# Optimization experiments

Hardware: AMD Instinct MI355X
Metric: run time of the kernel (lower is better)

Reference implementation:

```python
import jax, jax.numpy as jnp
import numpy as np

B, NF, NT = 8, 4096, 4096
D_IN, D_HID, D_OUT, D_V = 3, 128, 32, 16


def mlp(x, W1, b1, W2, b2):
    # x: [B, N, D_IN] -> [B, N, D_OUT]
    h = jax.nn.relu(jnp.einsum('bni,ih->bnh', x, W1) + b1)
    return jnp.einsum('bnh,ho->bno', h, W2) + b2


def l1_cdist(a, b):
    # a: [B, N, d], b: [B, M, d] -> [B, N, M], sum_d |a-b|
    # scan over the small feature dim d to avoid a [B,N,M,d] intermediate
    aT = jnp.moveaxis(a, -1, 0)  # [d, B, N]
    bT = jnp.moveaxis(b, -1, 0)  # [d, B, M]

    def step(acc, ab):
        ai, bi = ab
        return acc + jnp.abs(ai[:, :, None] - bi[:, None, :]), None

    init = jnp.zeros((a.shape[0], a.shape[1], b.shape[1]), dtype=a.dtype)
    acc, _ = jax.lax.scan(step, init, (aT, bT))
    return acc


def setup_inputs() -> dict:
    key = jax.random.key(0)
    ks = jax.random.split(key, 11)
    s1 = 1.0 / np.sqrt(D_IN)
    s2 = 1.0 / np.sqrt(D_HID)
    return {
        'coords_f': jax.random.normal(ks[0], (B, NF, D_IN), jnp.float32),
        'values_f': jax.random.normal(ks[1], (B, NF, D_V), jnp.float32),
        'coords_t': jax.random.normal(ks[2], (B, NT, D_IN), jnp.float32),
        'Wk1': jax.random.uniform(ks[3], (D_IN, D_HID), jnp.float32, -s1, s1),
        'bk1': jax.random.uniform(ks[4], (D_HID,), jnp.float32, -s1, s1),
        'Wk2': jax.random.uniform(ks[5], (D_HID, D_OUT), jnp.float32, -s2, s2),
        'bk2': jax.random.uniform(ks[6], (D_OUT,), jnp.float32, -s2, s2),
        'Wq1': jax.random.uniform(ks[7], (D_IN, D_HID), jnp.float32, -s1, s1),
        'bq1': jax.random.uniform(ks[8], (D_HID,), jnp.float32, -s1, s1),
        'Wq2': jax.random.uniform(ks[9], (D_HID, D_OUT), jnp.float32, -s2, s2),
        'bq2': jax.random.uniform(ks[10], (D_OUT,), jnp.float32, -s2, s2),
    }


def reference(coords_f, values_f, coords_t, Wk1, bk1, Wk2, bk2, Wq1, bq1, Wq2, bq2):
    Wk = mlp(coords_f, Wk1, bk1, Wk2, bk2)  # [B, NF, D_OUT]
    Wq = mlp(coords_t, Wq1, bq1, Wq2, bq2)  # [B, NT, D_OUT]
    score = l1_cdist(Wk, Wq)                # [B, NF, NT]
    attn = jax.nn.softmax(-(score ** 2) / 2.0, axis=1)  # softmax over NF
    # 'bij,bik->bjk': [B,NF,NT] x [B,NF,V] -> [B,NT,V]
    return jnp.einsum('bij,bik->bjk', attn, values_f)
```

## Files before the change

kernel.cpp:

```cpp
#include <hip/hip_runtime.h>

#define B 8
#define NF 4096
#define NT 4096
#define D_HID 128
#define D_OUT 32
#define D_V 16
#define TILE_I 64

__device__ inline float fast_exp2(float x) {
#if __has_builtin(__builtin_amdgcn_exp2f)
  return __builtin_amdgcn_exp2f(x);
#else
  return exp2f(x);
#endif
}

__global__ __launch_bounds__(256) void mlp_kernel(
    const float* __restrict__ x, const float* __restrict__ W1,
    const float* __restrict__ b1, const float* __restrict__ W2,
    const float* __restrict__ b2, float* __restrict__ out) {
  __shared__ float sW1[3 * D_HID];
  __shared__ float sb1[D_HID];
  __shared__ float sW2[D_HID * D_OUT];
  __shared__ float sb2[D_OUT];
  const int tid = threadIdx.x;
  for (int idx = tid; idx < D_HID * D_OUT; idx += 256) sW2[idx] = W2[idx];
  for (int idx = tid; idx < 3 * D_HID; idx += 256) sW1[idx] = W1[idx];
  if (tid < D_HID) sb1[tid] = b1[tid];
  if (tid < D_OUT) sb2[tid] = b2[tid];
  __syncthreads();

  const int t = blockIdx.x * 256 + tid;
  const float x0 = x[t * 3 + 0];
  const float x1 = x[t * 3 + 1];
  const float x2 = x[t * 3 + 2];
  float acc[D_OUT];
#pragma unroll
  for (int o = 0; o < D_OUT; ++o) acc[o] = sb2[o];
#pragma unroll 4
  for (int h = 0; h < D_HID; ++h) {
    float hv = fmaf(x2, sW1[2 * D_HID + h],
               fmaf(x1, sW1[1 * D_HID + h],
               fmaf(x0, sW1[0 * D_HID + h], sb1[h])));
    hv = fmaxf(hv, 0.0f);
    const float4* w2r = reinterpret_cast<const float4*>(&sW2[h * D_OUT]);
#pragma unroll
    for (int o4 = 0; o4 < D_OUT / 4; ++o4) {
      const float4 w = w2r[o4];
      acc[o4 * 4 + 0] = fmaf(hv, w.x, acc[o4 * 4 + 0]);
      acc[o4 * 4 + 1] = fmaf(hv, w.y, acc[o4 * 4 + 1]);
      acc[o4 * 4 + 2] = fmaf(hv, w.z, acc[o4 * 4 + 2]);
      acc[o4 * 4 + 3] = fmaf(hv, w.w, acc[o4 * 4 + 3]);
    }
  }
  float* op = out + (size_t)t * D_OUT;
#pragma unroll
  for (int o = 0; o < D_OUT; o += 4) {
    float4 w = make_float4(acc[o], acc[o + 1], acc[o + 2], acc[o + 3]);
    *reinterpret_cast<float4*>(op + o) = w;
  }
}

__global__ __launch_bounds__(256, 4) void attn_kernel(
    const float* __restrict__ Wk, const float* __restrict__ Wq,
    const float* __restrict__ Vf, float* __restrict__ partial,
    int nchunks, int chlen) {
  __shared__ float4 sTile[2][768];
  const int tid = threadIdx.x;
  const int j = blockIdx.x * 256 + tid;
  const int b = blockIdx.y;
  const int c = blockIdx.z;
  const int i0 = c * chlen;
  const int ntiles = chlen / TILE_I;

  const float* qp = Wq + ((size_t)b * NT + j) * D_OUT;
  float q[D_OUT];
#pragma unroll
  for (int d = 0; d < D_OUT; d += 4) {
    float4 t4 = *reinterpret_cast<const float4*>(qp + d);
    q[d + 0] = t4.x; q[d + 1] = t4.y; q[d + 2] = t4.z; q[d + 3] = t4.w;
  }

  constexpr float C2 = -0.72134752044448170368f;

  float m = -1e30f;
  float l = 0.0f;
  float acc[D_V];
#pragma unroll
  for (int k = 0; k < D_V; ++k) acc[k] = 0.0f;

  const float4* gK4 = reinterpret_cast<const float4*>(Wk + ((size_t)b * NF + i0) * D_OUT);
  const float4* gV4 = reinterpret_cast<const float4*>(Vf + ((size_t)b * NF + i0) * D_V);

  {
    float4 f0 = gK4[tid];
    float4 f1 = gK4[256 + tid];
    float4 f2 = gV4[tid];
    sTile[0][tid] = f0;
    sTile[0][256 + tid] = f1;
    sTile[0][512 + tid] = f2;
  }
  __syncthreads();

  for (int t = 0; t < ntiles; ++t) {
    const int cur = t & 1;
    float4 f0, f1, f2;
    const bool more = (t + 1 < ntiles);
    if (more) {
      f0 = gK4[(size_t)(t + 1) * 512 + tid];
      f1 = gK4[(size_t)(t + 1) * 512 + 256 + tid];
      f2 = gV4[(size_t)(t + 1) * 256 + tid];
    }
    const float4* kb4 = &sTile[cur][0];
    const float4* vb4 = &sTile[cur][512];
    for (int r = 0; r < TILE_I; ++r) {
      const float4 k0 = kb4[0];
      const float4 k1 = kb4[1];
      const float4 k2 = kb4[2];
      const float4 k3 = kb4[3];
      const float4 k4 = kb4[4];
      const float4 k5 = kb4[5];
      const float4 k6 = kb4[6];
      const float4 k7 = kb4[7];
      kb4 += 8;

      float a0 = fabsf(k0.x - q[0]);
      float a1 = fabsf(k0.y - q[1]);
      float a2 = fabsf(k0.z - q[2]);
      float a3 = fabsf(k0.w - q[3]);
      a0 += fabsf(k1.x - q[4]);
      a1 += fabsf(k1.y - q[5]);
      a2 += fabsf(k1.z - q[6]);
      a3 += fabsf(k1.w - q[7]);
      a0 += fabsf(k2.x - q[8]);
      a1 += fabsf(k2.y - q[9]);
      a2 += fabsf(k2.z - q[10]);
      a3 += fabsf(k2.w - q[11]);
      a0 += fabsf(k3.x - q[12]);
      a1 += fabsf(k3.y - q[13]);
      a2 += fabsf(k3.z - q[14]);
      a3 += fabsf(k3.w - q[15]);
      a0 += fabsf(k4.x - q[16]);
      a1 += fabsf(k4.y - q[17]);
      a2 += fabsf(k4.z - q[18]);
      a3 += fabsf(k4.w - q[19]);
      a0 += fabsf(k5.x - q[20]);
      a1 += fabsf(k5.y - q[21]);
      a2 += fabsf(k5.z - q[22]);
      a3 += fabsf(k5.w - q[23]);
      a0 += fabsf(k6.x - q[24]);
      a1 += fabsf(k6.y - q[25]);
      a2 += fabsf(k6.z - q[26]);
      a3 += fabsf(k6.w - q[27]);
      a0 += fabsf(k7.x - q[28]);
      a1 += fabsf(k7.y - q[29]);
      a2 += fabsf(k7.z - q[30]);
      a3 += fabsf(k7.w - q[31]);
      const float dist = (a0 + a1) + (a2 + a3);

      const float d2 = dist * dist;
      float parg = fmaf(C2, d2, -m);
      if (__any(parg > 4.0f)) {
        const float s2 = C2 * d2;
        const float mn = fmaxf(m, s2);
        const float al = fast_exp2(m - mn);
        l *= al;
#pragma unroll
        for (int k = 0; k < D_V; ++k) acc[k] *= al;
        m = mn;
        parg = s2 - m;
      }
      const float p = fast_exp2(parg);

      const float4 v0 = vb4[0];
      const float4 v1 = vb4[1];
      const float4 v2 = vb4[2];
      const float4 v3 = vb4[3];
      vb4 += 4;

      l += p;
      acc[0]  = fmaf(p, v0.x, acc[0]);
      acc[1]  = fmaf(p, v0.y, acc[1]);
      acc[2]  = fmaf(p, v0.z, acc[2]);
      acc[3]  = fmaf(p, v0.w, acc[3]);
      acc[4]  = fmaf(p, v1.x, acc[4]);
      acc[5]  = fmaf(p, v1.y, acc[5]);
      acc[6]  = fmaf(p, v1.z, acc[6]);
      acc[7]  = fmaf(p, v1.w, acc[7]);
      acc[8]  = fmaf(p, v2.x, acc[8]);
      acc[9]  = fmaf(p, v2.y, acc[9]);
      acc[10] = fmaf(p, v2.z, acc[10]);
      acc[11] = fmaf(p, v2.w, acc[11]);
      acc[12] = fmaf(p, v3.x, acc[12]);
      acc[13] = fmaf(p, v3.y, acc[13]);
      acc[14] = fmaf(p, v3.z, acc[14]);
      acc[15] = fmaf(p, v3.w, acc[15]);
    }
    if (more) {
      const int nxt = cur ^ 1;
      sTile[nxt][tid] = f0;
      sTile[nxt][256 + tid] = f1;
      sTile[nxt][512 + tid] = f2;
    }
    __syncthreads();
  }

  const size_t fstride = (size_t)nchunks * B * NT;
  float* ps = partial + ((size_t)c * B + b) * NT + j;
  ps[0] = m;
  ps[fstride] = l;
#pragma unroll
  for (int k = 0; k < D_V; ++k) ps[(size_t)(2 + k) * fstride] = acc[k];
}

__global__ __launch_bounds__(256) void combine_kernel(
    const float* __restrict__ partial, float* __restrict__ out, int nchunks) {
  const int t = blockIdx.x * 256 + threadIdx.x;
  const size_t fstride = (size_t)nchunks * B * NT;
  float M = -1e30f;
  for (int c = 0; c < nchunks; ++c)
    M = fmaxf(M, partial[(size_t)c * (B * NT) + t]);
  float L = 0.0f;
  float acc[D_V];
#pragma unroll
  for (int k = 0; k < D_V; ++k) acc[k] = 0.0f;
  for (int c = 0; c < nchunks; ++c) {
    const size_t base = (size_t)c * (B * NT) + t;
    const float w = fast_exp2(partial[base] - M);
    L = fmaf(w, partial[fstride + base], L);
#pragma unroll
    for (int k = 0; k < D_V; ++k)
      acc[k] = fmaf(w, partial[(size_t)(2 + k) * fstride + base], acc[k]);
  }
  const float inv = 1.0f / L;
  float* op = out + (size_t)t * D_V;
#pragma unroll
  for (int k = 0; k < D_V; ++k) op[k] = acc[k] * inv;
}

extern "C" void kernel_launch(void* const* d_in, const int* in_sizes, int n_in,
                              void* d_out, int out_size, void* d_ws, size_t ws_size,
                              hipStream_t stream) {
  const float* coords_f = (const float*)d_in[0];
  const float* values_f = (const float*)d_in[1];
  const float* coords_t = (const float*)d_in[2];
  const float* Wk1 = (const float*)d_in[3];
  const float* bk1 = (const float*)d_in[4];
  const float* Wk2 = (const float*)d_in[5];
  const float* bk2 = (const float*)d_in[6];
  const float* Wq1 = (const float*)d_in[7];
  const float* bq1 = (const float*)d_in[8];
  const float* Wq2 = (const float*)d_in[9];
  const float* bq2 = (const float*)d_in[10];
  float* out = (float*)d_out;

  float* Wk = (float*)d_ws;
  float* Wq = Wk + (size_t)B * NF * D_OUT;
  float* partial = Wq + (size_t)B * NT * D_OUT;

  const size_t fixed = (size_t)(B * NF * D_OUT + B * NT * D_OUT) * sizeof(float);
  int nchunks = 32;
  while (nchunks > 1 &&
         fixed + (size_t)B * NT * nchunks * 18 * sizeof(float) > ws_size)
    nchunks >>= 1;
  const int chlen = NF / nchunks;

  hipLaunchKernelGGL(mlp_kernel, dim3(B * NF / 256), dim3(256), 0, stream,
                     coords_f, Wk1, bk1, Wk2, bk2, Wk);
  hipLaunchKernelGGL(mlp_kernel, dim3(B * NT / 256), dim3(256), 0, stream,
                     coords_t, Wq1, bq1, Wq2, bq2, Wq);
  hipLaunchKernelGGL(attn_kernel, dim3(NT / 256, B, nchunks), dim3(256), 0, stream,
                     Wk, Wq, values_f, partial, nchunks, chlen);
  hipLaunchKernelGGL(combine_kernel, dim3(B * NT / 256), dim3(256), 0, stream,
                     partial, out, nchunks);
}
```

Baseline: 460.9 us.

## Process two query columns per thread in attention kernel; shrink MLP blocks

Each attention thread now handles two target points, so every K/V value read from shared memory is reused for two distance and accumulate chains. This halves LDS traffic per unit of work and the number of blocks. The cost is higher register pressure (occupancy hint lowered from 4 to 3 waves) and half as many blocks in the grid. The MLP kernel is also relaunched with 64-thread blocks, giving more blocks at the cost of loading the weights into shared memory more often.

```diff
diff --git a/kernel.cpp b/kernel.cpp
--- a/kernel.cpp
+++ b/kernel.cpp
@@ -16,7 +16,7 @@
 #endif
 }
 
-__global__ __launch_bounds__(256) void mlp_kernel(
+__global__ __launch_bounds__(64) void mlp_kernel(
     const float* __restrict__ x, const float* __restrict__ W1,
     const float* __restrict__ b1, const float* __restrict__ W2,
     const float* __restrict__ b2, float* __restrict__ out) {
@@ -25,13 +25,13 @@
   __shared__ float sW2[D_HID * D_OUT];
   __shared__ float sb2[D_OUT];
   const int tid = threadIdx.x;
-  for (int idx = tid; idx < D_HID * D_OUT; idx += 256) sW2[idx] = W2[idx];
-  for (int idx = tid; idx < 3 * D_HID; idx += 256) sW1[idx] = W1[idx];
-  if (tid < D_HID) sb1[tid] = b1[tid];
+  for (int idx = tid; idx < D_HID * D_OUT; idx += 64) sW2[idx] = W2[idx];
+  for (int idx = tid; idx < 3 * D_HID; idx += 64) sW1[idx] = W1[idx];
+  for (int idx = tid; idx < D_HID; idx += 64) sb1[idx] = b1[idx];
   if (tid < D_OUT) sb2[tid] = b2[tid];
   __syncthreads();
 
-  const int t = blockIdx.x * 256 + tid;
+  const int t = blockIdx.x * 64 + tid;
   const float x0 = x[t * 3 + 0];
   const float x1 = x[t * 3 + 1];
   const float x2 = x[t * 3 + 2];
@@ -62,33 +62,41 @@
   }
 }
 
-__global__ __launch_bounds__(256, 4) void attn_kernel(
+__global__ __launch_bounds__(256, 3) void attn_kernel(
     const float* __restrict__ Wk, const float* __restrict__ Wq,
     const float* __restrict__ Vf, float* __restrict__ partial,
     int nchunks, int chlen) {
   __shared__ float4 sTile[2][768];
   const int tid = threadIdx.x;
-  const int j = blockIdx.x * 256 + tid;
+  const int j0 = blockIdx.x * 512 + tid;
+  const int j1 = j0 + 256;
   const int b = blockIdx.y;
   const int c = blockIdx.z;
   const int i0 = c * chlen;
   const int ntiles = chlen / TILE_I;
 
-  const float* qp = Wq + ((size_t)b * NT + j) * D_OUT;
-  float q[D_OUT];
-#pragma unroll
-  for (int d = 0; d < D_OUT; d += 4) {
-    float4 t4 = *reinterpret_cast<const float4*>(qp + d);
-    q[d + 0] = t4.x; q[d + 1] = t4.y; q[d + 2] = t4.z; q[d + 3] = t4.w;
+  float q[2][D_OUT];
+  {
+    const float* qp0 = Wq + ((size_t)b * NT + j0) * D_OUT;
+    const float* qp1 = Wq + ((size_t)b * NT + j1) * D_OUT;
+#pragma unroll
+    for (int d = 0; d < D_OUT; d += 4) {
+      float4 t4 = *reinterpret_cast<const float4*>(qp0 + d);
+      q[0][d + 0] = t4.x; q[0][d + 1] = t4.y; q[0][d + 2] = t4.z; q[0][d + 3] = t4.w;
+      float4 u4 = *reinterpret_cast<const float4*>(qp1 + d);
+      q[1][d + 0] = u4.x; q[1][d + 1] = u4.y; q[1][d + 2] = u4.z; q[1][d + 3] = u4.w;
+    }
   }
 
   constexpr float C2 = -0.72134752044448170368f;
 
-  float m = -1e30f;
-  float l = 0.0f;
-  float acc[D_V];
-#pragma unroll
-  for (int k = 0; k < D_V; ++k) acc[k] = 0.0f;
+  float m[2] = {-1e30f, -1e30f};
+  float l[2] = {0.0f, 0.0f};
+  float acc[2][D_V];
+#pragma unroll
+  for (int s = 0; s < 2; ++s)
+#pragma unroll
+    for (int k = 0; k < D_V; ++k) acc[s][k] = 0.0f;
 
   const float4* gK4 = reinterpret_cast<const float4*>(Wk + ((size_t)b * NF + i0) * D_OUT);
   const float4* gV4 = reinterpret_cast<const float4*>(Vf + ((size_t)b * NF + i0) * D_V);
@@ -125,53 +133,69 @@
       const float4 k7 = kb4[7];
       kb4 += 8;
 
-      float a0 = fabsf(k0.x - q[0]);
-      float a1 = fabsf(k0.y - q[1]);
-      float a2 = fabsf(k0.z - q[2]);
-      float a3 = fabsf(k0.w - q[3]);
-      a0 += fabsf(k1.x - q[4]);
-      a1 += fabsf(k1.y - q[5]);
-      a2 += fabsf(k1.z - q[6]);
-      a3 += fabsf(k1.w - q[7]);
-      a0 += fabsf(k2.x - q[8]);
-      a1 += fabsf(k2.y - q[9]);
-      a2 += fabsf(k2.z - q[10]);
-      a3 += fabsf(k2.w - q[11]);
-      a0 += fabsf(k3.x - q[12]);
-      a1 += fabsf(k3.y - q[13]);
-      a2 += fabsf(k3.z - q[14]);
-      a3 += fabsf(k3.w - q[15]);
-      a0 += fabsf(k4.x - q[16]);
-      a1 += fabsf(k4.y - q[17]);
-      a2 += fabsf(k4.z - q[18]);
-      a3 += fabsf(k4.w - q[19]);
-      a0 += fabsf(k5.x - q[20]);
-      a1 += fabsf(k5.y - q[21]);
-      a2 += fabsf(k5.z - q[22]);
-      a3 += fabsf(k5.w - q[23]);
-      a0 += fabsf(k6.x - q[24]);
-      a1 += fabsf(k6.y - q[25]);
-      a2 += fabsf(k6.z - q[26]);
-      a3 += fabsf(k6.w - q[27]);
-      a0 += fabsf(k7.x - q[28]);
-      a1 += fabsf(k7.y - q[29]);
-      a2 += fabsf(k7.z - q[30]);
-      a3 += fabsf(k7.w - q[31]);
-      const float dist = (a0 + a1) + (a2 + a3);
-
-      const float d2 = dist * dist;
-      float parg = fmaf(C2, d2, -m);
-      if (__any(parg > 4.0f)) {
-        const float s2 = C2 * d2;
-        const float mn = fmaxf(m, s2);
-        const float al = fast_exp2(m - mn);
-        l *= al;
-#pragma unroll
-        for (int k = 0; k < D_V; ++k) acc[k] *= al;
-        m = mn;
-        parg = s2 - m;
+      float a0 = fabsf(k0.x - q[0][0]);
+      float b0 = fabsf(k0.x - q[1][0]);
+      float a1 = fabsf(k0.y - q[0][1]);
+      float b1 = fabsf(k0.y - q[1][1]);
+      float a2 = fabsf(k0.z - q[0][2]);
+      float b2 = fabsf(k0.z - q[1][2]);
+      float a3 = fabsf(k0.w - q[0][3]);
+      float b3 = fabsf(k0.w - q[1][3]);
+      a0 += fabsf(k1.x - q[0][4]);  b0 += fabsf(k1.x - q[1][4]);
+      a1 += fabsf(k1.y - q[0][5]);  b1 += fabsf(k1.y - q[1][5]);
+      a2 += fabsf(k1.z - q[0][6]);  b2 += fabsf(k1.z - q[1][6]);
+      a3 += fabsf(k1.w - q[0][7]);  b3 += fabsf(k1.w - q[1][7]);
+      a0 += fabsf(k2.x - q[0][8]);  b0 += fabsf(k2.x - q[1][8]);
+      a1 += fabsf(k2.y - q[0][9]);  b1 += fabsf(k2.y - q[1][9]);
+      a2 += fabsf(k2.z - q[0][10]); b2 += fabsf(k2.z - q[1][10]);
+      a3 += fabsf(k2.w - q[0][11]); b3 += fabsf(k2.w - q[1][11]);
+      a0 += fabsf(k3.x - q[0][12]); b0 += fabsf(k3.x - q[1][12]);
+      a1 += fabsf(k3.y - q[0][13]); b1 += fabsf(k3.y - q[1][13]);
+      a2 += fabsf(k3.z - q[0][14]); b2 += fabsf(k3.z - q[1][14]);
+      a3 += fabsf(k3.w - q[0][15]); b3 += fabsf(k3.w - q[1][15]);
+      a0 += fabsf(k4.x - q[0][16]); b0 += fabsf(k4.x - q[1][16]);
+      a1 += fabsf(k4.y - q[0][17]); b1 += fabsf(k4.y - q[1][17]);
+      a2 += fabsf(k4.z - q[0][18]); b2 += fabsf(k4.z - q[1][18]);
+      a3 += fabsf(k4.w - q[0][19]); b3 += fabsf(k4.w - q[1][19]);
+      a0 += fabsf(k5.x - q[0][20]); b0 += fabsf(k5.x - q[1][20]);
+      a1 += fabsf(k5.y - q[0][21]); b1 += fabsf(k5.y - q[1][21]);
+      a2 += fabsf(k5.z - q[0][22]); b2 += fabsf(k5.z - q[1][22]);
+      a3 += fabsf(k5.w - q[0][23]); b3 += fabsf(k5.w - q[1][23]);
+      a0 += fabsf(k6.x - q[0][24]); b0 += fabsf(k6.x - q[1][24]);
+      a1 += fabsf(k6.y - q[0][25]); b1 += fabsf(k6.y - q[1][25]);
+      a2 += fabsf(k6.z - q[0][26]); b2 += fabsf(k6.z - q[1][26]);
+      a3 += fabsf(k6.w - q[0][27]); b3 += fabsf(k6.w - q[1][27]);
+      a0 += fabsf(k7.x - q[0][28]); b0 += fabsf(k7.x - q[1][28]);
+      a1 += fabsf(k7.y - q[0][29]); b1 += fabsf(k7.y - q[1][29]);
+      a2 += fabsf(k7.z - q[0][30]); b2 += fabsf(k7.z - q[1][30]);
+      a3 += fabsf(k7.w - q[0][31]); b3 += fabsf(k7.w - q[1][31]);
+      const float dist0 = (a0 + a1) + (a2 + a3);
+      const float dist1 = (b0 + b1) + (b2 + b3);
+
+      const float d20 = dist0 * dist0;
+      const float d21 = dist1 * dist1;
+      float parg0 = fmaf(C2, d20, -m[0]);
+      float parg1 = fmaf(C2, d21, -m[1]);
+      if (__any(fmaxf(parg0, parg1) > 4.0f)) {
+        const float s20 = C2 * d20;
+        const float mn0 = fmaxf(m[0], s20);
+        const float al0 = fast_exp2(m[0] - mn0);
+        l[0] *= al0;
+#pragma unroll
+        for (int k = 0; k < D_V; ++k) acc[0][k] *= al0;
+        m[0] = mn0;
+        parg0 = s20 - mn0;
+        const float s21 = C2 * d21;
+        const float mn1 = fmaxf(m[1], s21);
+        const float al1 = fast_exp2(m[1] - mn1);
+        l[1] *= al1;
+#pragma unroll
+        for (int k = 0; k < D_V; ++k) acc[1][k] *= al1;
+        m[1] = mn1;
+        parg1 = s21 - mn1;
       }
-      const float p = fast_exp2(parg);
+      const float p0 = fast_exp2(parg0);
+      const float p1 = fast_exp2(parg1);
 
       const float4 v0 = vb4[0];
       const float4 v1 = vb4[1];
@@ -179,23 +203,24 @@
       const float4 v3 = vb4[3];
       vb4 += 4;
 
-      l += p;
-      acc[0]  = fmaf(p, v0.x, acc[0]);
-      acc[1]  = fmaf(p, v0.y, acc[1]);
-      acc[2]  = fmaf(p, v0.z, acc[2]);
-      acc[3]  = fmaf(p, v0.w, acc[3]);
-      acc[4]  = fmaf(p, v1.x, acc[4]);
-      acc[5]  = fmaf(p, v1.y, acc[5]);
-      acc[6]  = fmaf(p, v1.z, acc[6]);
-      acc[7]  = fmaf(p, v1.w, acc[7]);
-      acc[8]  = fmaf(p, v2.x, acc[8]);
-      acc[9]  = fmaf(p, v2.y, acc[9]);
-      acc[10] = fmaf(p, v2.z, acc[10]);
-      acc[11] = fmaf(p, v2.w, acc[11]);
-      acc[12] = fmaf(p, v3.x, acc[12]);
-      acc[13] = fmaf(p, v3.y, acc[13]);
-      acc[14] = fmaf(p, v3.z, acc[14]);
-      acc[15] = fmaf(p, v3.w, acc[15]);
+      l[0] += p0;
+      l[1] += p1;
+      acc[0][0]  = fmaf(p0, v0.x, acc[0][0]);   acc[1][0]  = fmaf(p1, v0.x, acc[1][0]);
+      acc[0][1]  = fmaf(p0, v0.y, acc[0][1]);   acc[1][1]  = fmaf(p1, v0.y, acc[1][1]);
+      acc[0][2]  = fmaf(p0, v0.z, acc[0][2]);   acc[1][2]  = fmaf(p1, v0.z, acc[1][2]);
+      acc[0][3]  = fmaf(p0, v0.w, acc[0][3]);   acc[1][3]  = fmaf(p1, v0.w, acc[1][3]);
+      acc[0][4]  = fmaf(p0, v1.x, acc[0][4]);   acc[1][4]  = fmaf(p1, v1.x, acc[1][4]);
+      acc[0][5]  = fmaf(p0, v1.y, acc[0][5]);   acc[1][5]  = fmaf(p1, v1.y, acc[1][5]);
+      acc[0][6]  = fmaf(p0, v1.z, acc[0][6]);   acc[1][6]  = fmaf(p1, v1.z, acc[1][6]);
+      acc[0][7]  = fmaf(p0, v1.w, acc[0][7]);   acc[1][7]  = fmaf(p1, v1.w, acc[1][7]);
+      acc[0][8]  = fmaf(p0, v2.x, acc[0][8]);   acc[1][8]  = fmaf(p1, v2.x, acc[1][8]);
+      acc[0][9]  = fmaf(p0, v2.y, acc[0][9]);   acc[1][9]  = fmaf(p1, v2.y, acc[1][9]);
+      acc[0][10] = fmaf(p0, v2.z, acc[0][10]);  acc[1][10] = fmaf(p1, v2.z, acc[1][10]);
+      acc[0][11] = fmaf(p0, v2.w, acc[0][11]);  acc[1][11] = fmaf(p1, v2.w, acc[1][11]);
+      acc[0][12] = fmaf(p0, v3.x, acc[0][12]);  acc[1][12] = fmaf(p1, v3.x, acc[1][12]);
+      acc[0][13] = fmaf(p0, v3.y, acc[0][13]);  acc[1][13] = fmaf(p1, v3.y, acc[1][13]);
+      acc[0][14] = fmaf(p0, v3.z, acc[0][14]);  acc[1][14] = fmaf(p1, v3.z, acc[1][14]);
+      acc[0][15] = fmaf(p0, v3.w, acc[0][15]);  acc[1][15] = fmaf(p1, v3.w, acc[1][15]);
     }
     if (more) {
       const int nxt = cur ^ 1;
@@ -207,11 +232,17 @@
   }
 
   const size_t fstride = (size_t)nchunks * B * NT;
-  float* ps = partial + ((size_t)c * B + b) * NT + j;
-  ps[0] = m;
-  ps[fstride] = l;
-#pragma unroll
-  for (int k = 0; k < D_V; ++k) ps[(size_t)(2 + k) * fstride] = acc[k];
+  float* ps0 = partial + ((size_t)c * B + b) * NT + j0;
+  float* ps1 = partial + ((size_t)c * B + b) * NT + j1;
+  ps0[0] = m[0];
+  ps1[0] = m[1];
+  ps0[fstride] = l[0];
+  ps1[fstride] = l[1];
+#pragma unroll
+  for (int k = 0; k < D_V; ++k) {
+    ps0[(size_t)(2 + k) * fstride] = acc[0][k];
+    ps1[(size_t)(2 + k) * fstride] = acc[1][k];
+  }
 }
 
 __global__ __launch_bounds__(256) void combine_kernel(
@@ -266,11 +297,11 @@
     nchunks >>= 1;
   const int chlen = NF / nchunks;
 
-  hipLaunchKernelGGL(mlp_kernel, dim3(B * NF / 256), dim3(256), 0, stream,
+  hipLaunchKernelGGL(mlp_kernel, dim3(B * NF / 64), dim3(64), 0, stream,
                      coords_f, Wk1, bk1, Wk2, bk2, Wk);
-  hipLaunchKernelGGL(mlp_kernel, dim3(B * NT / 256), dim3(256), 0, stream,
+  hipLaunchKernelGGL(mlp_kernel, dim3(B * NT / 64), dim3(64), 0, stream,
                      coords_t, Wq1, bq1, Wq2, bq2, Wq);
-  hipLaunchKernelGGL(attn_kernel, dim3(NT / 256, B, nchunks), dim3(256), 0, stream,
+  hipLaunchKernelGGL(attn_kernel, dim3(NT / 512, B, nchunks), dim3(256), 0, stream,
                      Wk, Wq, values_f, partial, nchunks, chlen);
   hipLaunchKernelGGL(combine_kernel, dim3(B * NT / 256), dim3(256), 0, stream,
                      partial, out, nchunks);
```

After: 428.4 us. -7.0%, faster.

## Register-tile four queries per thread pair with split feature dims in attention

Applied to the files above, without the earlier changes.

The attention kernel now has each pair of threads split the 32 feature dims and 16 value dims between them, and each thread handles four query columns. Every K/V row read from shared memory is therefore reused across four queries, and the partial distances are joined with a lane shuffle. Waves start at staggered row offsets to spread LDS bank accesses. The MLP kernels also move to 64-thread blocks. This cuts LDS traffic per FLOP, at the cost of more registers, lower occupancy (launch bound 3 instead of 4), an extra shuffle per row, and a shared rescale branch across four queries.

```diff
diff --git a/kernel.cpp b/kernel.cpp
--- a/kernel.cpp
+++ b/kernel.cpp
@@ -16,7 +16,7 @@
 #endif
 }
 
-__global__ __launch_bounds__(256) void mlp_kernel(
+__global__ __launch_bounds__(64) void mlp_kernel(
     const float* __restrict__ x, const float* __restrict__ W1,
     const float* __restrict__ b1, const float* __restrict__ W2,
     const float* __restrict__ b2, float* __restrict__ out) {
@@ -25,13 +25,13 @@
   __shared__ float sW2[D_HID * D_OUT];
   __shared__ float sb2[D_OUT];
   const int tid = threadIdx.x;
-  for (int idx = tid; idx < D_HID * D_OUT; idx += 256) sW2[idx] = W2[idx];
-  for (int idx = tid; idx < 3 * D_HID; idx += 256) sW1[idx] = W1[idx];
-  if (tid < D_HID) sb1[tid] = b1[tid];
+  for (int idx = tid; idx < D_HID * D_OUT; idx += 64) sW2[idx] = W2[idx];
+  for (int idx = tid; idx < 3 * D_HID; idx += 64) sW1[idx] = W1[idx];
+  for (int idx = tid; idx < D_HID; idx += 64) sb1[idx] = b1[idx];
   if (tid < D_OUT) sb2[tid] = b2[tid];
   __syncthreads();
 
-  const int t = blockIdx.x * 256 + tid;
+  const int t = blockIdx.x * 64 + tid;
   const float x0 = x[t * 3 + 0];
   const float x1 = x[t * 3 + 1];
   const float x2 = x[t * 3 + 2];
@@ -62,33 +62,45 @@
   }
 }
 
-__global__ __launch_bounds__(256, 4) void attn_kernel(
+__global__ __launch_bounds__(256, 3) void attn_kernel(
     const float* __restrict__ Wk, const float* __restrict__ Wq,
     const float* __restrict__ Vf, float* __restrict__ partial,
     int nchunks, int chlen) {
   __shared__ float4 sTile[2][768];
   const int tid = threadIdx.x;
-  const int j = blockIdx.x * 256 + tid;
+  const int pair = tid >> 1;
+  const int par = tid & 1;
+  const int wv = tid >> 6;
   const int b = blockIdx.y;
   const int c = blockIdx.z;
   const int i0 = c * chlen;
   const int ntiles = chlen / TILE_I;
-
-  const float* qp = Wq + ((size_t)b * NT + j) * D_OUT;
-  float q[D_OUT];
-#pragma unroll
-  for (int d = 0; d < D_OUT; d += 4) {
-    float4 t4 = *reinterpret_cast<const float4*>(qp + d);
-    q[d + 0] = t4.x; q[d + 1] = t4.y; q[d + 2] = t4.z; q[d + 3] = t4.w;
-  }
+  const int jbase = blockIdx.x * 512 + pair;
 
   constexpr float C2 = -0.72134752044448170368f;
 
-  float m = -1e30f;
-  float l = 0.0f;
-  float acc[D_V];
-#pragma unroll
-  for (int k = 0; k < D_V; ++k) acc[k] = 0.0f;
+  float q[4][16];
+#pragma unroll
+  for (int s = 0; s < 4; ++s) {
+    const float* qp = Wq + ((size_t)b * NT + jbase + s * 128) * D_OUT + par * 16;
+#pragma unroll
+    for (int d4 = 0; d4 < 4; ++d4) {
+      float4 t4 = *reinterpret_cast<const float4*>(qp + d4 * 4);
+      q[s][d4 * 4 + 0] = t4.x;
+      q[s][d4 * 4 + 1] = t4.y;
+      q[s][d4 * 4 + 2] = t4.z;
+      q[s][d4 * 4 + 3] = t4.w;
+    }
+  }
+
+  float m[4], l[4], acc[4][8];
+#pragma unroll
+  for (int s = 0; s < 4; ++s) {
+    m[s] = -1e30f;
+    l[s] = 0.0f;
+#pragma unroll
+    for (int k = 0; k < 8; ++k) acc[s][k] = 0.0f;
+  }
 
   const float4* gK4 = reinterpret_cast<const float4*>(Wk + ((size_t)b * NF + i0) * D_OUT);
   const float4* gV4 = reinterpret_cast<const float4*>(Vf + ((size_t)b * NF + i0) * D_V);
@@ -112,90 +124,77 @@
       f1 = gK4[(size_t)(t + 1) * 512 + 256 + tid];
       f2 = gV4[(size_t)(t + 1) * 256 + tid];
     }
-    const float4* kb4 = &sTile[cur][0];
-    const float4* vb4 = &sTile[cur][512];
-    for (int r = 0; r < TILE_I; ++r) {
-      const float4 k0 = kb4[0];
-      const float4 k1 = kb4[1];
-      const float4 k2 = kb4[2];
-      const float4 k3 = kb4[3];
-      const float4 k4 = kb4[4];
-      const float4 k5 = kb4[5];
-      const float4 k6 = kb4[6];
-      const float4 k7 = kb4[7];
-      kb4 += 8;
-
-      float a0 = fabsf(k0.x - q[0]);
-      float a1 = fabsf(k0.y - q[1]);
-      float a2 = fabsf(k0.z - q[2]);
-      float a3 = fabsf(k0.w - q[3]);
-      a0 += fabsf(k1.x - q[4]);
-      a1 += fabsf(k1.y - q[5]);
-      a2 += fabsf(k1.z - q[6]);
-      a3 += fabsf(k1.w - q[7]);
-      a0 += fabsf(k2.x - q[8]);
-      a1 += fabsf(k2.y - q[9]);
-      a2 += fabsf(k2.z - q[10]);
-      a3 += fabsf(k2.w - q[11]);
-      a0 += fabsf(k3.x - q[12]);
-      a1 += fabsf(k3.y - q[13]);
-      a2 += fabsf(k3.z - q[14]);
-      a3 += fabsf(k3.w - q[15]);
-      a0 += fabsf(k4.x - q[16]);
-      a1 += fabsf(k4.y - q[17]);
-      a2 += fabsf(k4.z - q[18]);
-      a3 += fabsf(k4.w - q[19]);
-      a0 += fabsf(k5.x - q[20]);
-      a1 += fabsf(k5.y - q[21]);
-      a2 += fabsf(k5.z - q[22]);
-      a3 += fabsf(k5.w - q[23]);
-      a0 += fabsf(k6.x - q[24]);
-      a1 += fabsf(k6.y - q[25]);
-      a2 += fabsf(k6.z - q[26]);
-      a3 += fabsf(k6.w - q[27]);
-      a0 += fabsf(k7.x - q[28]);
-      a1 += fabsf(k7.y - q[29]);
-      a2 += fabsf(k7.z - q[30]);
-      a3 += fabsf(k7.w - q[31]);
-      const float dist = (a0 + a1) + (a2 + a3);
-
-      const float d2 = dist * dist;
-      float parg = fmaf(C2, d2, -m);
-      if (__any(parg > 4.0f)) {
-        const float s2 = C2 * d2;
-        const float mn = fmaxf(m, s2);
-        const float al = fast_exp2(m - mn);
-        l *= al;
-#pragma unroll
-        for (int k = 0; k < D_V; ++k) acc[k] *= al;
-        m = mn;
-        parg = s2 - m;
-      }
-      const float p = fast_exp2(parg);
-
-      const float4 v0 = vb4[0];
-      const float4 v1 = vb4[1];
-      const float4 v2 = vb4[2];
-      const float4 v3 = vb4[3];
-      vb4 += 4;
-
-      l += p;
-      acc[0]  = fmaf(p, v0.x, acc[0]);
-      acc[1]  = fmaf(p, v0.y, acc[1]);
-      acc[2]  = fmaf(p, v0.z, acc[2]);
-      acc[3]  = fmaf(p, v0.w, acc[3]);
-      acc[4]  = fmaf(p, v1.x, acc[4]);
-      acc[5]  = fmaf(p, v1.y, acc[5]);
-      acc[6]  = fmaf(p, v1.z, acc[6]);
-      acc[7]  = fmaf(p, v1.w, acc[7]);
-      acc[8]  = fmaf(p, v2.x, acc[8]);
-      acc[9]  = fmaf(p, v2.y, acc[9]);
-      acc[10] = fmaf(p, v2.z, acc[10]);
-      acc[11] = fmaf(p, v2.w, acc[11]);
-      acc[12] = fmaf(p, v3.x, acc[12]);
-      acc[13] = fmaf(p, v3.y, acc[13]);
-      acc[14] = fmaf(p, v3.z, acc[14]);
-      acc[15] = fmaf(p, v3.w, acc[15]);
+    for (int rr = 0; rr < TILE_I; ++rr) {
+      const int r = (rr + (wv << 4)) & (TILE_I - 1);
+      const float4* kp = &sTile[cur][r * 8 + par * 4];
+      const float4 k0 = kp[0];
+      const float4 k1 = kp[1];
+      const float4 k2 = kp[2];
+      const float4 k3 = kp[3];
+
+      float pa[4];
+#pragma unroll
+      for (int s = 0; s < 4; ++s) {
+        float A = fabsf(k0.x - q[s][0]);
+        float Bb = fabsf(k0.y - q[s][1]);
+        A += fabsf(k0.z - q[s][2]);
+        Bb += fabsf(k0.w - q[s][3]);
+        A += fabsf(k1.x - q[s][4]);
+        Bb += fabsf(k1.y - q[s][5]);
+        A += fabsf(k1.z - q[s][6]);
+        Bb += fabsf(k1.w - q[s][7]);
+        A += fabsf(k2.x - q[s][8]);
+        Bb += fabsf(k2.y - q[s][9]);
+        A += fabsf(k2.z - q[s][10]);
+        Bb += fabsf(k2.w - q[s][11]);
+        A += fabsf(k3.x - q[s][12]);
+        Bb += fabsf(k3.y - q[s][13]);
+        A += fabsf(k3.z - q[s][14]);
+        Bb += fabsf(k3.w - q[s][15]);
+        pa[s] = A + Bb;
+      }
+
+      float s2[4], parg[4];
+#pragma unroll
+      for (int s = 0; s < 4; ++s) {
+        const float dist = pa[s] + __shfl_xor(pa[s], 1);
+        s2[s] = C2 * (dist * dist);
+        parg[s] = s2[s] - m[s];
+      }
+      const float mparg = fmaxf(fmaxf(parg[0], parg[1]), fmaxf(parg[2], parg[3]));
+      if (__any(mparg > 4.0f)) {
+#pragma unroll
+        for (int s = 0; s < 4; ++s) {
+          const float mn = fmaxf(m[s], s2[s]);
+          const float al = fast_exp2(m[s] - mn);
+          l[s] *= al;
+#pragma unroll
+          for (int k = 0; k < 8; ++k) acc[s][k] *= al;
+          m[s] = mn;
+          parg[s] = s2[s] - mn;
+        }
+      }
+      float p[4];
+#pragma unroll
+      for (int s = 0; s < 4; ++s) {
+        p[s] = fast_exp2(parg[s]);
+        l[s] += p[s];
+      }
+
+      const float4* vp = &sTile[cur][512 + r * 4 + par * 2];
+      const float4 v0 = vp[0];
+      const float4 v1 = vp[1];
+#pragma unroll
+      for (int s = 0; s < 4; ++s) {
+        acc[s][0] = fmaf(p[s], v0.x, acc[s][0]);
+        acc[s][1] = fmaf(p[s], v0.y, acc[s][1]);
+        acc[s][2] = fmaf(p[s], v0.z, acc[s][2]);
+        acc[s][3] = fmaf(p[s], v0.w, acc[s][3]);
+        acc[s][4] = fmaf(p[s], v1.x, acc[s][4]);
+        acc[s][5] = fmaf(p[s], v1.y, acc[s][5]);
+        acc[s][6] = fmaf(p[s], v1.z, acc[s][6]);
+        acc[s][7] = fmaf(p[s], v1.w, acc[s][7]);
+      }
     }
     if (more) {
       const int nxt = cur ^ 1;
@@ -207,11 +206,18 @@
   }
 
   const size_t fstride = (size_t)nchunks * B * NT;
-  float* ps = partial + ((size_t)c * B + b) * NT + j;
-  ps[0] = m;
-  ps[fstride] = l;
-#pragma unroll
-  for (int k = 0; k < D_V; ++k) ps[(size_t)(2 + k) * fstride] = acc[k];
+  const size_t base = ((size_t)c * B + b) * NT;
+#pragma unroll
+  for (int s = 0; s < 4; ++s) {
+    float* ps = partial + base + (jbase + s * 128);
+    if (par == 0) {
+      ps[0] = m[s];
+      ps[fstride] = l[s];
+    }
+#pragma unroll
+    for (int k = 0; k < 8; ++k)
+      ps[(size_t)(2 + par * 8 + k) * fstride] = acc[s][k];
+  }
 }
 
 __global__ __launch_bounds__(256) void combine_kernel(
@@ -266,11 +272,11 @@
     nchunks >>= 1;
   const int chlen = NF / nchunks;
 
-  hipLaunchKernelGGL(mlp_kernel, dim3(B * NF / 256), dim3(256), 0, stream,
+  hipLaunchKernelGGL(mlp_kernel, dim3(B * NF / 64), dim3(64), 0, stream,
                      coords_f, Wk1, bk1, Wk2, bk2, Wk);
-  hipLaunchKernelGGL(mlp_kernel, dim3(B * NT / 256), dim3(256), 0, stream,
+  hipLaunchKernelGGL(mlp_kernel, dim3(B * NT / 64), dim3(64), 0, stream,
                      coords_t, Wq1, bq1, Wq2, bq2, Wq);
-  hipLaunchKernelGGL(attn_kernel, dim3(NT / 256, B, nchunks), dim3(256), 0, stream,
+  hipLaunchKernelGGL(attn_kernel, dim3(NT / 512, B, nchunks), dim3(256), 0, stream,
                      Wk, Wq, values_f, partial, nchunks, chlen);
   hipLaunchKernelGGL(combine_kernel, dim3(B * NT / 256), dim3(256), 0, stream,
                      partial, out, nchunks);
```

After: 452.2 us. No clear change (-1.9%).
